# Kernel tuning notes

Hardware: AMD Instinct MI355X
Metric: run time of the kernel (lower is better)

## Reference

```python
import jax, jax.numpy as jnp
import numpy as np

B, T, U, V = 8, 512, 128, 128  # batch, frames, label len (U+1 pred steps), vocab incl. blank
BLANK = 0


def setup_inputs() -> dict:
    key = jax.random.key(0)
    k1, k2, k3, k4 = jax.random.split(key, 4)
    logits = jax.random.normal(k1, (B, T, U + 1, V), dtype=jnp.float32)
    y = jax.random.randint(k2, (B, U), 1, V).astype(jnp.int32)  # labels, never blank
    logit_lens = jax.random.randint(k3, (B,), T // 2, T + 1).astype(jnp.int32)
    y_lens = jax.random.randint(k4, (B,), U // 2, U + 1).astype(jnp.int32)
    batch_offset = jnp.cumsum(logit_lens * (y_lens + 1)).astype(jnp.int32)
    return {
        "logits": logits,
        "y": y,
        "logit_lens": logit_lens,
        "y_lens": y_lens,
        "batch_offset": batch_offset,
        "max_f_len": T,
    }


def _combine(e1, e2):
    # log-domain affine recurrence x[u] = logaddexp(x[u-1] + c[u], a[u])
    c1, a1 = e1
    c2, a2 = e2
    return (c1 + c2, jnp.logaddexp(a1 + c2, a2))


def rnnt_loss(logits, y, logit_lens, y_lens, blank_idx):
    Bb, Tt, U1, Vv = logits.shape
    Uu = U1 - 1
    lp = jax.nn.log_softmax(logits, axis=-1)            # [B,T,U+1,V]
    blank = lp[..., blank_idx]                          # [B,T,U+1]
    idx = jnp.broadcast_to(y[:, None, :, None], (Bb, Tt, Uu, 1)).astype(jnp.int32)
    emit = jnp.take_along_axis(lp[:, :, :Uu, :], idx, axis=3)[..., 0]  # [B,T,U]

    # alpha[0,u] = sum_{v<u} emit(0,v)
    row0 = jnp.concatenate(
        [jnp.zeros((Bb, 1), lp.dtype), jnp.cumsum(emit[:, 0, :], axis=1)], axis=1
    )  # [B,U+1]
    neg = jnp.full((Bb, 1), -jnp.inf, lp.dtype)

    def step(prev_row, x):
        bl_prev, em_t = x                               # [B,U+1], [B,U]
        a = prev_row + bl_prev                          # come-from-below (blank at t-1)
        c = jnp.concatenate([neg, em_t], axis=1)        # come-from-left (emit at t)
        _, row = jax.lax.associative_scan(_combine, (c, a), axis=1)
        return row, row

    xs = (jnp.swapaxes(blank[:, : Tt - 1, :], 0, 1), jnp.swapaxes(emit[:, 1:, :], 0, 1))
    _, rows = jax.lax.scan(step, row0, xs)              # [T-1,B,U+1]
    alphas = jnp.swapaxes(jnp.concatenate([row0[None], rows], axis=0), 0, 1)  # [B,T,U+1]

    bi = jnp.arange(Bb)
    ti = logit_lens - 1
    ui = y_lens
    ll = alphas[bi, ti, ui] + blank[bi, ti, ui]
    return -ll                                          # per-utterance negative log-lik


def reference(logits, y, logit_lens, y_lens, batch_offset, max_f_len):
    # batch_offset / max_f_len are packing metadata, unused when packed_input=False
    return rnnt_loss(logits, y, logit_lens, y_lens, BLANK).mean()
```

## Files before the change

### kernel.cpp

```cpp
#include <hip/hip_runtime.h>

#define Bb 8
#define Tt 512
#define Uu 128
#define U1 129
#define Vv 128

#define OUT_OFF 0
#define CTROWS 321
#define PCKROW 512
#define PCKBSZ ((size_t)CTROWS * PCKROW)
#define PCK_OFF ((size_t)Bb * Tt * U1 * 2)
#define CTCOL_OFF (PCK_OFF + (size_t)Bb * PCKBSZ)
#define WROWF 768
#define WROWS 160
#define WBSZ ((size_t)WROWS * WROWF)
#define W_OFF (CTCOL_OFF + (size_t)Bb * CTROWS * 4)
#define WCOL_OFF (W_OFF + (size_t)Bb * WBSZ)
#define WB_OFF (WCOL_OFF + (size_t)Bb * WROWS * 8)
#define ST_OFF (WB_OFF + (size_t)Bb * WBSZ)
#define RES_OFF (ST_OFF + (size_t)Bb * 260)

#define K_LN2    0.6931471805599453f
#define K_INVLN2 1.4426950408889634f
#define SENT (-1.0e30f)

__device__ __forceinline__ float fexp2(float x) {
    float r; asm("v_exp_f32 %0, %1" : "=v"(r) : "v"(x)); return r;
}
__device__ __forceinline__ float flog2(float x) {
    float r; asm("v_log_f32 %0, %1" : "=v"(r) : "v"(x)); return r;
}
__device__ __forceinline__ float fmax3(float x, float y, float z) {
    float r; asm("v_max3_f32 %0, %1, %2, %3" : "=v"(r) : "v"(x), "v"(y), "v"(z));
    return r;
}
__device__ __forceinline__ float lae2(float x, float y) {
    float dd = x - y;
    float nad = __builtin_bit_cast(float, __builtin_bit_cast(int, dd) | 0x80000000);
    return fmaxf(x, y) + flog2(1.0f + fexp2(nad));
}
__device__ __forceinline__ float lae3(float x, float y, float z) {
    float m = fmax3(x, y, z);
    return m + flog2(fexp2(x - m) + fexp2(y - m) + fexp2(z - m));
}
__device__ __forceinline__ float lae5(float a, float b, float c, float d, float e) {
    float m = fmax3(a, b, c);
    m = fmax3(m, d, e);
    return m + flog2(fexp2(a - m) + fexp2(b - m) + fexp2(c - m)
                   + fexp2(d - m) + fexp2(e - m));
}
__device__ __forceinline__ float lae6(float a, float b, float c, float d, float e, float f) {
    float m = fmaxf(fmax3(a, b, c), fmax3(d, e, f));
    return m + flog2(fexp2(a - m) + fexp2(b - m) + fexp2(c - m)
                   + fexp2(d - m) + fexp2(e - m) + fexp2(f - m));
}

__global__ __launch_bounds__(256) void lse_kernel(
    const float* __restrict__ logits, const int* __restrict__ y,
    const int* __restrict__ logit_lens, const int* __restrict__ y_lens,
    float* __restrict__ ws)
{
    const int b = blockIdx.y;
    const int t = blockIdx.x;
    if (t >= logit_lens[b]) return;
    const int Ue = y_lens[b];

    float2* outv = (float2*)(ws + OUT_OFF);
    const int wid  = threadIdx.x >> 6;
    const int lane = threadIdx.x & 63;
    const int g    = lane >> 4;
    const int gl   = lane & 15;
    const unsigned rowbase = ((unsigned)b * Tt + t) * U1;
    const int yb = b * Uu;

    for (int u0 = wid * 8; u0 <= Ue; u0 += 32) {
        const int ua = u0 + g;
        const int ub = u0 + 4 + g;
        const int uca = ua > Ue ? Ue : ua;
        const int ucb = ub > Ue ? Ue : ub;
        const float* pa = logits + (size_t)(rowbase + uca) * Vv;
        const float* pb = logits + (size_t)(rowbase + ucb) * Vv;
        float4 a1 = *(const float4*)(pa + gl * 4);
        float4 a2 = *(const float4*)(pa + 64 + gl * 4);
        float4 b1 = *(const float4*)(pb + gl * 4);
        float4 b2 = *(const float4*)(pb + 64 + gl * 4);

        float sa = (fexp2(a1.x * K_INVLN2) + fexp2(a1.y * K_INVLN2))
                 + (fexp2(a1.z * K_INVLN2) + fexp2(a1.w * K_INVLN2))
                 + (fexp2(a2.x * K_INVLN2) + fexp2(a2.y * K_INVLN2))
                 + (fexp2(a2.z * K_INVLN2) + fexp2(a2.w * K_INVLN2));
        float sb = (fexp2(b1.x * K_INVLN2) + fexp2(b1.y * K_INVLN2))
                 + (fexp2(b1.z * K_INVLN2) + fexp2(b1.w * K_INVLN2))
                 + (fexp2(b2.x * K_INVLN2) + fexp2(b2.y * K_INVLN2))
                 + (fexp2(b2.z * K_INVLN2) + fexp2(b2.w * K_INVLN2));
        #pragma unroll
        for (int off = 8; off; off >>= 1) {
            sa += __shfl_xor(sa, off);
            sb += __shfl_xor(sb, off);
        }
        float lseA = flog2(sa);
        float lseB = flog2(sb);

        float emA = SENT, emB = SENT;
        if (uca < Uu) {
            int yv = y[yb + uca];
            int c = yv & 3;
            float4 cv = (yv & 64) ? a2 : a1;
            float cand = (c == 0) ? cv.x : (c == 1) ? cv.y : (c == 2) ? cv.z : cv.w;
            float ev = __shfl(cand, (lane & 48) | ((yv & 63) >> 2));
            emA = ev * K_INVLN2 - lseA;
        }
        if (ucb < Uu) {
            int yv = y[yb + ucb];
            int c = yv & 3;
            float4 cv = (yv & 64) ? b2 : b1;
            float cand = (c == 0) ? cv.x : (c == 1) ? cv.y : (c == 2) ? cv.z : cv.w;
            float ev = __shfl(cand, (lane & 48) | ((yv & 63) >> 2));
            emB = ev * K_INVLN2 - lseB;
        }
        if (gl == 0) {
            if (ua <= Ue) outv[rowbase + ua] = make_float2(a1.x * K_INVLN2 - lseA, emA);
            if (ub <= Ue) outv[rowbase + ub] = make_float2(b1.x * K_INVLN2 - lseB, emB);
        }
    }
}

__global__ __launch_bounds__(256) void cond_kernel(
    const int* __restrict__ logit_lens, const int* __restrict__ y_lens,
    float* __restrict__ ws)
{
    const int b = blockIdx.x / 320;
    const int m = blockIdx.x - b * 320 + 1;
    if (m > ((logit_lens[b] - 1 + y_lens[b]) >> 1)) return;
    const int r1 = 2 * m - 2, r2 = 2 * m - 1;
    const float2* outv = (const float2*)(ws + OUT_OFF);

    __shared__ float2 D1[U1], D2[U1];
    __shared__ float pckS[PCKROW];
    for (int q = threadIdx.x; q < 2 * U1; q += 256) {
        const int which = q >= U1;
        const int j = q - which * U1;
        const int t = (which ? r2 : r1) - j;
        float2 val = make_float2(SENT, SENT);
        if (t >= 0 && t < Tt) val = outv[((size_t)b * Tt + t) * U1 + j];
        (which ? D2 : D1)[j] = val;
    }
    __syncthreads();

    const int u = threadIdx.x;
    if (u <= 128) {
        float2 d1  = D1[u], d2 = D2[u];
        float2 d1m = (u >= 1) ? D1[u - 1] : make_float2(SENT, SENT);
        float d2my  = (u >= 1) ? D2[u - 1].y : SENT;
        float d1m2y = (u >= 2) ? D1[u - 2].y : SENT;
        float A = d1.x + d2.x;
        float B = lae2(d1m.y + d2.x, d1m.x + d2my);
        float C = d1m2y + d2my;
        if (u < 128) {
            int base = (u >> 1) * 8 + (u & 1);
            pckS[base]     = A;
            pckS[base + 2] = B;
            pckS[base + 4] = C;
            if ((u & 1) == 0) { pckS[base + 6] = 0.0f; pckS[base + 7] = 0.0f; }
        } else {
            ((float4*)(ws + CTCOL_OFF))[(size_t)b * CTROWS + m] = make_float4(A, B, C, 0.0f);
        }
    }
    __syncthreads();

    float* pckG = ws + PCK_OFF + (size_t)b * PCKBSZ + (size_t)m * PCKROW;
    for (int i = threadIdx.x; i < PCKROW; i += 256) pckG[i] = pckS[i];
}

__global__ __launch_bounds__(256) void compose_kernel(
    const int* __restrict__ logit_lens, const int* __restrict__ y_lens,
    float* __restrict__ ws)
{
    const int b = blockIdx.x / 159;
    const int q = blockIdx.x - b * 159 + 1;
    const int dend = logit_lens[b] - 1 + y_lens[b];
    if (4 * q > dend) return;
    const int m1 = 2 * q - 1, m2 = 2 * q;
    const float* PCKb = ws + PCK_OFF + (size_t)b * PCKBSZ;
    const float4* COLb = (const float4*)(ws + CTCOL_OFF) + (size_t)b * CTROWS;

    __shared__ float a1s[131], b1s[131], c1s[131];
    __shared__ float wrk[WROWF], wrkB[WROWF];
    __shared__ float sW0[129], sW1[129], sW2[129], sW3[129], sW4[129];
    const int u = threadIdx.x;
    if (u < 2) { a1s[u] = SENT; b1s[u] = SENT; c1s[u] = SENT; }
    if (u < 128) {
        const float* p = PCKb + (size_t)m1 * PCKROW + (u >> 1) * 8;
        int par = u & 1;
        a1s[u + 2] = p[par]; b1s[u + 2] = p[2 + par]; c1s[u + 2] = p[4 + par];
    } else if (u == 128) {
        float4 cc = COLb[m1];
        a1s[130] = cc.x; b1s[130] = cc.y; c1s[130] = cc.z;
    }
    __syncthreads();

    if (u <= 128) {
        float A2, B2, C2;
        if (u < 128) {
            const float* p = PCKb + (size_t)m2 * PCKROW + (u >> 1) * 8;
            int par = u & 1;
            A2 = p[par]; B2 = p[2 + par]; C2 = p[4 + par];
        } else {
            float4 cc = COLb[m2];
            A2 = cc.x; B2 = cc.y; C2 = cc.z;
        }
        float A1 = a1s[u + 2], A1m = a1s[u + 1], A1m2 = a1s[u];
        float B1 = b1s[u + 2], B1m = b1s[u + 1], B1m2 = b1s[u];
        float C1 = c1s[u + 2], C1m = c1s[u + 1], C1m2 = c1s[u];
        float W0 = A2 + A1;
        float W1 = lae2(A2 + B1, B2 + A1m);
        float W2 = lae3(A2 + C1, B2 + B1m, C2 + A1m2);
        float W3 = lae2(B2 + C1m, C2 + B1m2);
        float W4 = C2 + C1m2;
        sW0[u] = W0; sW1[u] = W1; sW2[u] = W2; sW3[u] = W3; sW4[u] = W4;
        if (u < 128) {
            int base = (u >> 1) * 12 + (u & 1);
            wrk[base]     = W0;
            wrk[base + 2] = W1;
            wrk[base + 4] = W2;
            wrk[base + 6] = W3;
            wrk[base + 8] = W4;
            if ((u & 1) == 0) { wrk[base + 10] = 0.0f; wrk[base + 11] = 0.0f; }
        } else {
            float* wc = ws + WCOL_OFF + ((size_t)b * WROWS + q) * 8;
            wc[0] = W0; wc[1] = W1; wc[2] = W2; wc[3] = W3; wc[4] = W4;
            wc[5] = 0.0f; wc[6] = 0.0f; wc[7] = 0.0f;
        }
    }
    __syncthreads();

    if (u < 64) {
        const int l = u, e = 2 * l;
        float cx2 = (e + 2 <= 127) ? sW2[e + 2] : SENT;
        float cx3 = (e + 3 <= 127) ? sW3[e + 3] : SENT;
        float cx4 = (e + 4 <= 127) ? sW4[e + 4] : SENT;
        float cy1 = (e + 2 <= 127) ? sW1[e + 2] : SENT;
        float cy2 = (e + 3 <= 127) ? sW2[e + 3] : SENT;
        float cy3 = (e + 4 <= 127) ? sW3[e + 4] : SENT;
        float cy4 = (e + 5 <= 127) ? sW4[e + 5] : SENT;
        float c5x = (l == 62) ? sW4[128] : (l == 63) ? sW2[128] : SENT;
        float c5y = (l == 62) ? sW3[128] : (l == 63) ? sW1[128] : SENT;
        float* rb = wrkB + l * 12;
        rb[0] = sW0[e];     rb[1] = sW1[e + 1]; rb[2]  = cx2; rb[3]  = cx3;
        rb[4] = cx4;        rb[5] = sW0[e + 1]; rb[6]  = cy1; rb[7]  = cy2;
        rb[8] = cy3;        rb[9] = cy4;        rb[10] = c5x; rb[11] = c5y;
    }
    __syncthreads();

    float* wg  = ws + W_OFF  + (size_t)b * WBSZ + (size_t)q * WROWF;
    float* wbg = ws + WB_OFF + (size_t)b * WBSZ + (size_t)q * WROWF;
    for (int i = threadIdx.x; i < WROWF; i += 256) { wg[i] = wrk[i]; wbg[i] = wrkB[i]; }
}

template<int MODE>
__device__ __forceinline__ float rotU(float x, int lane) {
    if constexpr (MODE == 2) {
        return __shfl(x, (lane + 63) & 63);
    } else {
        constexpr int CTRL = (MODE == 0) ? 0x13C : 0x134;
        int i = __builtin_bit_cast(int, x);
        i = __builtin_amdgcn_update_dpp(i, i, CTRL, 0xF, 0xF, true);
        return __builtin_bit_cast(float, i);
    }
}
template<int MODE>
__device__ __forceinline__ float rotD(float x, int lane) {
    if constexpr (MODE == 2) {
        return __shfl(x, (lane + 1) & 63);
    } else {
        constexpr int CTRL = (MODE == 0) ? 0x134 : 0x13C;
        int i = __builtin_bit_cast(int, x);
        i = __builtin_amdgcn_update_dpp(i, i, CTRL, 0xF, 0xF, true);
        return __builtin_bit_cast(float, i);
    }
}

template<int MODE, bool H128>
__device__ __forceinline__ void fw_body(int b, int lane, int Tb, int Ub,
                                        float* __restrict__ ws)
{
    const float* WTb = ws + W_OFF + (size_t)b * WBSZ;
    const float* WCb = ws + WCOL_OFF + (size_t)b * WROWS * 8;
    int zv; asm volatile("v_mov_b32 %0, 0" : "=v"(zv));

    float px = (lane == 0) ? 0.0f : SENT;
    float py = SENT, p2 = SENT;
    const int dend = Tb - 1 + Ub;
    const int nq   = dend >> 2;
    const int qend = nq >> 1;

    float4 A0,A1,A2,A3,A4,A5,A6,A7;
    float4 B0,B1,B2,B3,B4,B5,B6,B7;
    float2 C0,C1,C2,C3,C4,C5,C6,C7;
    float4 Oa0,Oa1,Oa2,Oa3,Oa4,Oa5,Oa6,Oa7;
    float2 Oc0,Oc1,Oc2,Oc3,Oc4,Oc5,Oc6,Oc7;

#define LOADW(i, qq) { unsigned o = (unsigned)(qq) * WROWF + lane * 12; \
    A##i = *(const float4*)(WTb + o); \
    B##i = *(const float4*)(WTb + o + 4); \
    C##i = *(const float2*)(WTb + o + 8); \
    if constexpr (H128) { \
        Oa##i = *(const float4*)(WCb + (qq) * 8 + zv); \
        Oc##i = *(const float2*)(WCb + (qq) * 8 + 4 + zv); } }

#define PIN(i) if constexpr (H128) { \
        asm volatile("" : "+v"(A##i.x), "+v"(A##i.y), "+v"(A##i.z), "+v"(A##i.w), \
                          "+v"(B##i.x), "+v"(B##i.y), "+v"(B##i.z), "+v"(B##i.w), \
                          "+v"(C##i.x), "+v"(C##i.y), \
                          "+v"(Oa##i.x), "+v"(Oa##i.y), "+v"(Oa##i.z), "+v"(Oa##i.w), \
                          "+v"(Oc##i.x)); \
    } else { \
        asm volatile("" : "+v"(A##i.x), "+v"(A##i.y), "+v"(A##i.z), "+v"(A##i.w), \
                          "+v"(B##i.x), "+v"(B##i.y), "+v"(B##i.z), "+v"(B##i.w), \
                          "+v"(C##i.x), "+v"(C##i.y)); \
    }

#define COMP4(i) { \
    float p1y = rotU<MODE>(py, lane); \
    float p1x = rotU<MODE>(px, lane); \
    float p2y = rotU<MODE>(p1y, lane); \
    float p2x = rotU<MODE>(p1x, lane); \
    float nx = lae5(px + A##i.x, p1y + A##i.z, p1x + B##i.x, p2y + B##i.z, p2x + C##i.x); \
    float ny = lae5(py + A##i.y, px + A##i.w, p1y + B##i.y, p1x + B##i.w, p2y + C##i.y); \
    if constexpr (H128) p2 = lae5(p2 + Oa##i.x, p1y + Oa##i.y, p1x + Oa##i.z, \
                                  p2y + Oa##i.w, p2x + Oc##i.x); \
    px = nx; py = ny; }

    LOADW(0,1) LOADW(1,2) LOADW(2,3) LOADW(3,4)
    LOADW(4,5) LOADW(5,6) LOADW(6,7) LOADW(7,8)

    int q = 1;
    for (; q + 7 <= qend; q += 8) {
        PIN(0) COMP4(0) { int dn = q + 8  > qend ? qend : q + 8;  LOADW(0, dn) }
        PIN(1) COMP4(1) { int dn = q + 9  > qend ? qend : q + 9;  LOADW(1, dn) }
        PIN(2) COMP4(2) { int dn = q + 10 > qend ? qend : q + 10; LOADW(2, dn) }
        PIN(3) COMP4(3) { int dn = q + 11 > qend ? qend : q + 11; LOADW(3, dn) }
        PIN(4) COMP4(4) { int dn = q + 12 > qend ? qend : q + 12; LOADW(4, dn) }
        PIN(5) COMP4(5) { int dn = q + 13 > qend ? qend : q + 13; LOADW(5, dn) }
        PIN(6) COMP4(6) { int dn = q + 14 > qend ? qend : q + 14; LOADW(6, dn) }
        PIN(7) COMP4(7) { int dn = q + 15 > qend ? qend : q + 15; LOADW(7, dn) }
    }
#define TAILW(i) if (q <= qend) { PIN(i) COMP4(i) q++; }
    TAILW(0) TAILW(1) TAILW(2) TAILW(3) TAILW(4) TAILW(5) TAILW(6)

    float* F = ws + ST_OFF + (size_t)b * 260;
    ((float2*)F)[lane] = make_float2(px, py);
    if (lane == 0) F[128] = H128 ? p2 : SENT;
#undef LOADW
#undef PIN
#undef COMP4
#undef TAILW
}

template<int MODE>
__device__ __forceinline__ void bw_body(int b, int lane, int Tb, int Ub,
                                        float* __restrict__ ws)
{
    const float2* outv = (const float2*)(ws + OUT_OFF);
    const float* PCKb = ws + PCK_OFF + (size_t)b * PCKBSZ;
    const float4* COLb = (const float4*)(ws + CTCOL_OFF) + (size_t)b * CTROWS;
    const float* WBb = ws + WB_OFF + (size_t)b * WBSZ;
    const float* WCb = ws + WCOL_OFF + (size_t)b * WROWS * 8;
    int zv; asm volatile("v_mov_b32 %0, 0" : "=v"(zv));

    const int dend = Tb - 1 + Ub;
    const int nq   = dend >> 2;
    const int qlo  = (nq >> 1) + 1;
    const int rem  = dend & 3;

    float wx = SENT, wy = SENT, w128 = SENT;
    if (Ub == 128) w128 = 0.0f;
    else if (lane == (Ub >> 1)) { if (Ub & 1) wy = 0.0f; else wx = 0.0f; }

    float4 X0,X1,X2,X3,X4,X5,X6,X7;
    float4 Y0,Y1,Y2,Y3,Y4,Y5,Y6,Y7;
    float4 Z0,Z1,Z2,Z3,Z4,Z5,Z6,Z7;
    float w0c0,w0c1,w0c2,w0c3,w0c4,w0c5,w0c6,w0c7;

#define LOADB(i, qq) { unsigned o = (unsigned)(qq) * WROWF + lane * 12; \
    X##i = *(const float4*)(WBb + o); \
    Y##i = *(const float4*)(WBb + o + 4); \
    Z##i = *(const float4*)(WBb + o + 8); \
    w0c##i = *(WCb + (qq) * 8 + zv); }

#define PINB(i) asm volatile("" : "+v"(X##i.x), "+v"(X##i.y), "+v"(X##i.z), "+v"(X##i.w), \
                          "+v"(Y##i.x), "+v"(Y##i.y), "+v"(Y##i.z), "+v"(Y##i.w), \
                          "+v"(Z##i.x), "+v"(Z##i.y), "+v"(Z##i.z), "+v"(Z##i.w), \
                          "+v"(w0c##i));

#define CLD(v) ((v) < qlo ? qlo : (v))
    LOADB(0, CLD(nq))     LOADB(1, CLD(nq - 1)) LOADB(2, CLD(nq - 2)) LOADB(3, CLD(nq - 3))
    LOADB(4, CLD(nq - 4)) LOADB(5, CLD(nq - 5)) LOADB(6, CLD(nq - 6)) LOADB(7, CLD(nq - 7))

    if (rem & 1) {
        const int r = dend - 1;
        int j1 = 2 * lane, j2 = 2 * lane + 1;
        int t1 = r - j1; t1 = t1 > Tt - 1 ? Tt - 1 : t1; if (t1 < 0) t1 = 0;
        int t2 = r - j2; t2 = t2 > Tt - 1 ? Tt - 1 : t2; if (t2 < 0) t2 = 0;
        float2 F1 = outv[((size_t)b * Tt + t1) * U1 + j1];
        float2 F2 = outv[((size_t)b * Tt + t2) * U1 + j2];
        int tg = r - 128; if (tg < 0) tg = 0;
        float2 G = outv[((size_t)b * Tt + tg) * U1 + 128];
        float n1x = rotD<MODE>(wx, lane);
        float nx = lae2(F1.x + wx, F1.y + wy);
        float ny = lae2(F2.x + wy, F2.y + ((lane == 63) ? w128 : n1x));
        w128 = G.x + w128;
        wx = nx; wy = ny;
    }
    if (rem >= 2) {
        const int mpair = 2 * nq + 1;
        const float* prow = PCKb + (size_t)mpair * PCKROW;
        float4 Qp  = *(const float4*)(prow + (lane << 3));
        float2 Rp  = *(const float2*)(prow + (lane << 3) + 4);
        int lp = lane + 1 > 63 ? 63 : lane + 1;
        float4 QpN = *(const float4*)(prow + (lp << 3));
        float2 RpN = *(const float2*)(prow + (lp << 3) + 4);
        float4 Op  = COLb[mpair + zv];
        float n1x = rotD<MODE>(wx, lane), n1y = rotD<MODE>(wy, lane);
        float nx = lae3(Qp.x + wx, Qp.w + wy,
                        (lane == 63) ? (Op.z + w128) : (RpN.x + n1x));
        float ny = lae3(Qp.y + wy,
                        (lane == 63) ? (Op.y + w128) : (QpN.z + n1x),
                        (lane == 63) ? SENT : (RpN.y + n1y));
        w128 = Op.x + w128;
        wx = nx; wy = ny;
    }

#define COMPB(i) { \
    float n1x = rotD<MODE>(wx, lane), n1y = rotD<MODE>(wy, lane); \
    float n2x = rotD<MODE>(n1x, lane), n2y = rotD<MODE>(n1y, lane); \
    float nx = lae6(wx + X##i.x, wy + X##i.y, n1x + X##i.z, n1y + X##i.w, \
                    n2x + Y##i.x, Z##i.z + w128); \
    float ny = lae6(wy + Y##i.y, n1x + Y##i.z, n1y + Y##i.w, n2x + Z##i.x, \
                    n2y + Z##i.y, Z##i.w + w128); \
    w128 = w0c##i + w128; \
    wx = nx; wy = ny; }

    int q = nq;
    for (; q - 7 >= qlo; q -= 8) {
        PINB(0) COMPB(0) LOADB(0, CLD(q - 8))
        PINB(1) COMPB(1) LOADB(1, CLD(q - 9))
        PINB(2) COMPB(2) LOADB(2, CLD(q - 10))
        PINB(3) COMPB(3) LOADB(3, CLD(q - 11))
        PINB(4) COMPB(4) LOADB(4, CLD(q - 12))
        PINB(5) COMPB(5) LOADB(5, CLD(q - 13))
        PINB(6) COMPB(6) LOADB(6, CLD(q - 14))
        PINB(7) COMPB(7) LOADB(7, CLD(q - 15))
    }
#define TAILB(i) if (q >= qlo) { PINB(i) COMPB(i) q--; }
    TAILB(0) TAILB(1) TAILB(2) TAILB(3) TAILB(4) TAILB(5) TAILB(6)

    float* Bst = ws + ST_OFF + (size_t)b * 260 + 130;
    ((float2*)Bst)[lane] = make_float2(wx, wy);
    if (lane == 0) Bst[128] = w128;
#undef LOADB
#undef PINB
#undef CLD
#undef COMPB
#undef TAILB
}

__global__ __launch_bounds__(64) void dp_kernel(
    const int* __restrict__ logit_lens, const int* __restrict__ y_lens,
    float* __restrict__ ws)
{
    const int b   = blockIdx.x >> 1;
    const int dir = blockIdx.x & 1;
    const int lane = threadIdx.x;
    const int Tb = logit_lens[b];
    const int Ub = y_lens[b];
    const bool h = (Ub == 128);
    int li = lane;
    int r0 = __builtin_amdgcn_update_dpp(li, li, 0x13C, 0xF, 0xF, true);
    int r1 = __builtin_amdgcn_update_dpp(li, li, 0x134, 0xF, 0xF, true);
    int wantU = (lane + 63) & 63, wantD = (lane + 1) & 63;
    int mode = 2;
    if (__all(r0 == wantU) && __all(r1 == wantD)) mode = 0;
    else if (__all(r1 == wantU) && __all(r0 == wantD)) mode = 1;

    if (dir == 0) {
        if (mode == 0)      { if (h) fw_body<0, true>(b, lane, Tb, Ub, ws); else fw_body<0, false>(b, lane, Tb, Ub, ws); }
        else if (mode == 1) { if (h) fw_body<1, true>(b, lane, Tb, Ub, ws); else fw_body<1, false>(b, lane, Tb, Ub, ws); }
        else                { if (h) fw_body<2, true>(b, lane, Tb, Ub, ws); else fw_body<2, false>(b, lane, Tb, Ub, ws); }
    } else {
        if (mode == 0)      bw_body<0>(b, lane, Tb, Ub, ws);
        else if (mode == 1) bw_body<1>(b, lane, Tb, Ub, ws);
        else                bw_body<2>(b, lane, Tb, Ub, ws);
    }
}

__global__ __launch_bounds__(64) void combine_kernel(
    const int* __restrict__ logit_lens, const int* __restrict__ y_lens,
    float* __restrict__ ws)
{
    const int b = blockIdx.x;
    const int lane = threadIdx.x;
    const float* F = ws + ST_OFF + (size_t)b * 260;
    const float* Bs = F + 130;
    float2 v = ((const float2*)F)[lane];
    float2 w = ((const float2*)Bs)[lane];
    float r = lae2(v.x + w.x, v.y + w.y);
    #pragma unroll
    for (int off = 32; off; off >>= 1)
        r = lae2(r, __shfl_xor(r, off));
    r = lae2(r, F[128] + Bs[128]);
    const int Tb = logit_lens[b], Ub = y_lens[b];
    const float2* outv = (const float2*)(ws + OUT_OFF);
    float pbf = outv[((size_t)b * Tt + (Tb - 1)) * U1 + Ub].x;
    if (lane == 0)
        ws[RES_OFF + b] = -(r + pbf) * K_LN2;
}

__global__ void mean_kernel(const float* __restrict__ res, float* __restrict__ out)
{
    if (threadIdx.x == 0) {
        float s = 0.0f;
        #pragma unroll
        for (int i = 0; i < Bb; ++i) s += res[i];
        out[0] = s * (1.0f / Bb);
    }
}

extern "C" void kernel_launch(void* const* d_in, const int* in_sizes, int n_in,
                              void* d_out, int out_size, void* d_ws, size_t ws_size,
                              hipStream_t stream) {
    const float* logits     = (const float*)d_in[0];
    const int*   y          = (const int*)d_in[1];
    const int*   logit_lens = (const int*)d_in[2];
    const int*   y_lens     = (const int*)d_in[3];
    float* ws  = (float*)d_ws;
    float* out = (float*)d_out;

    dim3 lgrid(Tt, Bb);
    lse_kernel<<<lgrid, 256, 0, stream>>>(logits, y, logit_lens, y_lens, ws);
    cond_kernel<<<Bb * 320, 256, 0, stream>>>(logit_lens, y_lens, ws);
    compose_kernel<<<Bb * 159, 256, 0, stream>>>(logit_lens, y_lens, ws);
    dp_kernel<<<Bb * 2, 64, 0, stream>>>(logit_lens, y_lens, ws);
    combine_kernel<<<Bb, 64, 0, stream>>>(logit_lens, y_lens, ws);
    mean_kernel<<<1, 64, 0, stream>>>(ws + RES_OFF, out);
}
```

Before: 64.54 us.

## Fuse cond kernel into compose and rebalance forward/backward split point

Removes the separate cond_kernel by having each compose block load four diagonal rows of the lse output and compute both pair transition matrices in shared memory, writing the packed pair only for the trailing odd block. This drops a kernel launch and the global round trip of the packed pair data. The forward/backward meeting point is also moved from half to 8/15 of the quad count, rebalancing the two dp waves, and WROWS grows to 161 to fit the extra compose block.

```diff
diff --git a/kernel.cpp b/kernel.cpp
--- a/kernel.cpp
+++ b/kernel.cpp
@@ -13,7 +13,7 @@
 #define PCK_OFF ((size_t)Bb * Tt * U1 * 2)
 #define CTCOL_OFF (PCK_OFF + (size_t)Bb * PCKBSZ)
 #define WROWF 768
-#define WROWS 160
+#define WROWS 161
 #define WBSZ ((size_t)WROWS * WROWF)
 #define W_OFF (CTCOL_OFF + (size_t)Bb * CTROWS * 4)
 #define WCOL_OFF (W_OFF + (size_t)Bb * WBSZ)
@@ -126,98 +126,84 @@
     }
 }
 
-__global__ __launch_bounds__(256) void cond_kernel(
-    const int* __restrict__ logit_lens, const int* __restrict__ y_lens,
-    float* __restrict__ ws)
-{
-    const int b = blockIdx.x / 320;
-    const int m = blockIdx.x - b * 320 + 1;
-    if (m > ((logit_lens[b] - 1 + y_lens[b]) >> 1)) return;
-    const int r1 = 2 * m - 2, r2 = 2 * m - 1;
-    const float2* outv = (const float2*)(ws + OUT_OFF);
-
-    __shared__ float2 D1[U1], D2[U1];
-    __shared__ float pckS[PCKROW];
-    for (int q = threadIdx.x; q < 2 * U1; q += 256) {
-        const int which = q >= U1;
-        const int j = q - which * U1;
-        const int t = (which ? r2 : r1) - j;
-        float2 val = make_float2(SENT, SENT);
-        if (t >= 0 && t < Tt) val = outv[((size_t)b * Tt + t) * U1 + j];
-        (which ? D2 : D1)[j] = val;
-    }
-    __syncthreads();
-
-    const int u = threadIdx.x;
-    if (u <= 128) {
-        float2 d1  = D1[u], d2 = D2[u];
-        float2 d1m = (u >= 1) ? D1[u - 1] : make_float2(SENT, SENT);
-        float d2my  = (u >= 1) ? D2[u - 1].y : SENT;
-        float d1m2y = (u >= 2) ? D1[u - 2].y : SENT;
-        float A = d1.x + d2.x;
-        float B = lae2(d1m.y + d2.x, d1m.x + d2my);
-        float C = d1m2y + d2my;
-        if (u < 128) {
-            int base = (u >> 1) * 8 + (u & 1);
-            pckS[base]     = A;
-            pckS[base + 2] = B;
-            pckS[base + 4] = C;
-            if ((u & 1) == 0) { pckS[base + 6] = 0.0f; pckS[base + 7] = 0.0f; }
-        } else {
-            ((float4*)(ws + CTCOL_OFF))[(size_t)b * CTROWS + m] = make_float4(A, B, C, 0.0f);
-        }
-    }
-    __syncthreads();
-
-    float* pckG = ws + PCK_OFF + (size_t)b * PCKBSZ + (size_t)m * PCKROW;
-    for (int i = threadIdx.x; i < PCKROW; i += 256) pckG[i] = pckS[i];
-}
-
 __global__ __launch_bounds__(256) void compose_kernel(
     const int* __restrict__ logit_lens, const int* __restrict__ y_lens,
     float* __restrict__ ws)
 {
-    const int b = blockIdx.x / 159;
-    const int q = blockIdx.x - b * 159 + 1;
+    const int b = blockIdx.x / 160;
+    const int q = blockIdx.x - b * 160 + 1;
     const int dend = logit_lens[b] - 1 + y_lens[b];
-    if (4 * q > dend) return;
-    const int m1 = 2 * q - 1, m2 = 2 * q;
-    const float* PCKb = ws + PCK_OFF + (size_t)b * PCKBSZ;
-    const float4* COLb = (const float4*)(ws + CTCOL_OFF) + (size_t)b * CTROWS;
-
+    const int nq = dend >> 2;
+    const bool full = (4 * q <= dend);
+    const bool pair_only = (!full) && (q == nq + 1);
+    if (!full && !pair_only) return;
+    const float2* outv = (const float2*)(ws + OUT_OFF);
+
+    __shared__ float2 D[4][U1];
     __shared__ float a1s[131], b1s[131], c1s[131];
     __shared__ float wrk[WROWF], wrkB[WROWF];
     __shared__ float sW0[129], sW1[129], sW2[129], sW3[129], sW4[129];
+    __shared__ float pckS[PCKROW];
     const int u = threadIdx.x;
+
+    for (int i = threadIdx.x; i < 4 * U1; i += 256) {
+        int row = i / U1, j = i - row * U1;
+        int r = 4 * (q - 1) + row;
+        int t = r - j;
+        D[row][j] = (t >= 0 && t < Tt) ? outv[((size_t)b * Tt + t) * U1 + j]
+                                       : make_float2(SENT, SENT);
+    }
+    __syncthreads();
+
+    float A2r = SENT, B2r = SENT, C2r = SENT;
     if (u < 2) { a1s[u] = SENT; b1s[u] = SENT; c1s[u] = SENT; }
-    if (u < 128) {
-        const float* p = PCKb + (size_t)m1 * PCKROW + (u >> 1) * 8;
-        int par = u & 1;
-        a1s[u + 2] = p[par]; b1s[u + 2] = p[2 + par]; c1s[u + 2] = p[4 + par];
-    } else if (u == 128) {
-        float4 cc = COLb[m1];
-        a1s[130] = cc.x; b1s[130] = cc.y; c1s[130] = cc.z;
+    if (u <= 128) {
+        float2 d1 = D[0][u], d2 = D[1][u];
+        float2 d1m = (u >= 1) ? D[0][u - 1] : make_float2(SENT, SENT);
+        float d2my  = (u >= 1) ? D[1][u - 1].y : SENT;
+        float d1m2y = (u >= 2) ? D[0][u - 2].y : SENT;
+        a1s[u + 2] = d1.x + d2.x;
+        b1s[u + 2] = lae2(d1m.y + d2.x, d1m.x + d2my);
+        c1s[u + 2] = d1m2y + d2my;
+        float2 e1 = D[2][u], e2 = D[3][u];
+        float2 e1m = (u >= 1) ? D[2][u - 1] : make_float2(SENT, SENT);
+        float e2my  = (u >= 1) ? D[3][u - 1].y : SENT;
+        float e1m2y = (u >= 2) ? D[2][u - 2].y : SENT;
+        A2r = e1.x + e2.x;
+        B2r = lae2(e1m.y + e2.x, e1m.x + e2my);
+        C2r = e1m2y + e2my;
     }
     __syncthreads();
 
+    if (pair_only) {
+        if (u <= 128) {
+            float A = a1s[u + 2], B = b1s[u + 2], C = c1s[u + 2];
+            if (u < 128) {
+                int base = (u >> 1) * 8 + (u & 1);
+                pckS[base]     = A;
+                pckS[base + 2] = B;
+                pckS[base + 4] = C;
+                if ((u & 1) == 0) { pckS[base + 6] = 0.0f; pckS[base + 7] = 0.0f; }
+            } else {
+                ((float4*)(ws + CTCOL_OFF))[(size_t)b * CTROWS + (2 * q - 1)]
+                    = make_float4(A, B, C, 0.0f);
+            }
+        }
+        __syncthreads();
+        float* pckG = ws + PCK_OFF + (size_t)b * PCKBSZ + (size_t)(2 * q - 1) * PCKROW;
+        for (int i = threadIdx.x; i < PCKROW; i += 256) pckG[i] = pckS[i];
+        return;
+    }
+
     if (u <= 128) {
-        float A2, B2, C2;
-        if (u < 128) {
-            const float* p = PCKb + (size_t)m2 * PCKROW + (u >> 1) * 8;
-            int par = u & 1;
-            A2 = p[par]; B2 = p[2 + par]; C2 = p[4 + par];
-        } else {
-            float4 cc = COLb[m2];
-            A2 = cc.x; B2 = cc.y; C2 = cc.z;
-        }
         float A1 = a1s[u + 2], A1m = a1s[u + 1], A1m2 = a1s[u];
         float B1 = b1s[u + 2], B1m = b1s[u + 1], B1m2 = b1s[u];
         float C1 = c1s[u + 2], C1m = c1s[u + 1], C1m2 = c1s[u];
-        float W0 = A2 + A1;
-        float W1 = lae2(A2 + B1, B2 + A1m);
-        float W2 = lae3(A2 + C1, B2 + B1m, C2 + A1m2);
-        float W3 = lae2(B2 + C1m, C2 + B1m2);
-        float W4 = C2 + C1m2;
+        float W0 = A2r + A1;
+        float W1 = lae2(A2r + B1, B2r + A1m);
+        float W2 = lae3(A2r + C1, B2r + B1m, C2r + A1m2);
+        float W3 = lae2(B2r + C1m, C2r + B1m2);
+        float W4 = C2r + C1m2;
         sW0[u] = W0; sW1[u] = W1; sW2[u] = W2; sW3[u] = W3; sW4[u] = W4;
         if (u < 128) {
             int base = (u >> 1) * 12 + (u & 1);
@@ -293,7 +279,7 @@
     float py = SENT, p2 = SENT;
     const int dend = Tb - 1 + Ub;
     const int nq   = dend >> 2;
-    const int qend = nq >> 1;
+    const int qend = (nq * 8) / 15;
 
     float4 A0,A1,A2,A3,A4,A5,A6,A7;
     float4 B0,B1,B2,B3,B4,B5,B6,B7;
@@ -371,7 +357,7 @@
 
     const int dend = Tb - 1 + Ub;
     const int nq   = dend >> 2;
-    const int qlo  = (nq >> 1) + 1;
+    const int qlo  = (nq * 8) / 15 + 1;
     const int rem  = dend & 3;
 
     float wx = SENT, wy = SENT, w128 = SENT;
@@ -539,8 +525,7 @@
 
     dim3 lgrid(Tt, Bb);
     lse_kernel<<<lgrid, 256, 0, stream>>>(logits, y, logit_lens, y_lens, ws);
-    cond_kernel<<<Bb * 320, 256, 0, stream>>>(logit_lens, y_lens, ws);
-    compose_kernel<<<Bb * 159, 256, 0, stream>>>(logit_lens, y_lens, ws);
+    compose_kernel<<<Bb * 160, 256, 0, stream>>>(logit_lens, y_lens, ws);
     dp_kernel<<<Bb * 2, 64, 0, stream>>>(logit_lens, y_lens, ws);
     combine_kernel<<<Bb, 64, 0, stream>>>(logit_lens, y_lens, ws);
     mean_kernel<<<1, 64, 0, stream>>>(ws + RES_OFF, out);
```

Result: faster. 58.30 us (-9.7%).
